# Kernel optimization log

Measured on AMD Instinct MI355X. Metric: run time of the kernel, lower is better.

## Reference

```python
import jax, jax.numpy as jnp
import numpy as np

IMG = 512
STRIDES = (8.0, 16.0, 32.0)   # p3, p4, p5
ROI = 7                        # roi_size
SR = 2                         # roi_align sampling ratio (fixed; torchvision default -1 is adaptive)
IOU_LOW, IOU_HIGH = 0.4, 0.6   # fg/bg matching thresholds (2nd-stage)
NUM_CLASSES = 20
B, R, M, C = 4, 256, 40, 256


def _make_boxes(key, b, n, max_wh):
    k1, k2 = jax.random.split(key)
    cxy = jax.random.uniform(k1, (b, n, 2), minval=0.0, maxval=float(IMG))
    wh = jax.random.uniform(k2, (b, n, 2), minval=16.0, maxval=float(max_wh))
    x1y1 = jnp.clip(cxy - wh / 2, 0.0, IMG - 1.0)
    x2y2 = jnp.clip(cxy + wh / 2, x1y1 + 1.0, float(IMG))
    return jnp.concatenate([x1y1, x2y2], axis=-1)


def setup_inputs() -> dict:
    key = jax.random.key(0)
    ks = jax.random.split(key, 12)
    feats_p3 = jax.random.normal(ks[0], (B, C, 64, 64), jnp.float32)
    feats_p4 = jax.random.normal(ks[1], (B, C, 32, 32), jnp.float32)
    feats_p5 = jax.random.normal(ks[2], (B, C, 16, 16), jnp.float32)
    props_p3 = _make_boxes(ks[3], B, R, 128)
    props_p4 = _make_boxes(ks[4], B, R, 256)
    props_p5 = _make_boxes(ks[5], B, R, 512)
    gt_xyxy = _make_boxes(ks[6], B, M, 400)
    gt_cls = jax.random.randint(ks[7], (B, M, 1), 0, NUM_CLASSES).astype(jnp.float32)
    gt = jnp.concatenate([gt_xyxy, gt_cls], axis=-1)
    pad = (jnp.arange(M) >= 25)[None, :, None]   # last 15 rows are padding (class -1)
    gt_boxes = jnp.where(pad, -1.0, gt)
    conv_w = jax.random.normal(ks[8], (C, C, 3, 3), jnp.float32) * 0.01
    conv_b = jnp.zeros((C,), jnp.float32)
    fc_w = jax.random.normal(ks[9], (NUM_CLASSES + 1, C * ROI * ROI), jnp.float32) * 0.01
    fc_b = jnp.zeros((NUM_CLASSES + 1,), jnp.float32)
    return {"feats_p3": feats_p3, "feats_p4": feats_p4, "feats_p5": feats_p5,
            "props_p3": props_p3, "props_p4": props_p4, "props_p5": props_p5,
            "gt_boxes": gt_boxes, "conv_w": conv_w, "conv_b": conv_b,
            "fc_w": fc_w, "fc_b": fc_b}


def _bilinear(feat, ys, xs):
    # feat: (C,H,W); ys: (R,G,1); xs: (R,1,G) -> (C,R,G,G)
    Cc, H, W = feat.shape
    valid = (ys >= -1.0) & (ys <= H) & (xs >= -1.0) & (xs <= W)
    y = jnp.clip(ys, 0.0, H - 1.0)
    x = jnp.clip(xs, 0.0, W - 1.0)
    y0f = jnp.floor(y); x0f = jnp.floor(x)
    y0 = y0f.astype(jnp.int32); x0 = x0f.astype(jnp.int32)
    y1 = jnp.minimum(y0 + 1, H - 1); x1 = jnp.minimum(x0 + 1, W - 1)
    ly = y - y0f; lx = x - x0f
    hy = 1.0 - ly; hx = 1.0 - lx
    v = (feat[:, y0, x0] * (hy * hx) + feat[:, y0, x1] * (hy * lx)
         + feat[:, y1, x0] * (ly * hx) + feat[:, y1, x1] * (ly * lx))
    return jnp.where(valid, v, 0.0)


def _roi_align(feat, rois, scale):
    # feat: (C,H,W); rois: (R,4) xyxy in image coords; aligned=True
    r = rois.shape[0]
    x1 = rois[:, 0] * scale - 0.5
    y1 = rois[:, 1] * scale - 0.5
    roi_w = rois[:, 2] * scale - 0.5 - x1
    roi_h = rois[:, 3] * scale - 0.5 - y1
    G = ROI * SR
    frac = (jnp.arange(G, dtype=feat.dtype) + 0.5) / G
    xs = x1[:, None] + frac[None, :] * roi_w[:, None]   # (R,G)
    ys = y1[:, None] + frac[None, :] * roi_h[:, None]
    v = _bilinear(feat, ys[:, :, None], xs[:, None, :])  # (C,R,G,G)
    v = v.transpose(1, 0, 2, 3).reshape(r, -1, ROI, SR, ROI, SR)
    return v.mean(axis=(3, 5))                            # (R,C,7,7)


def _iou(b1, b2):
    # b1: (N,4), b2: (M,4) -> (N,M)
    tl = jnp.maximum(b1[:, None, :2], b2[None, :, :2])
    br = jnp.minimum(b1[:, None, 2:4], b2[None, :, 2:4])
    inter = jnp.clip(br - tl, 0.0).prod(-1)
    a1 = (b1[:, 2:4] - b1[:, :2]).prod(-1)
    a2 = (b2[:, 2:4] - b2[:, :2]).prod(-1)
    return inter / (a1[:, None] + a2[None, :] - inter)


def _match(props, gt):
    # props: (N,4); gt: (M,5) padded with class -1
    valid = gt[:, 4] != -1
    m = jnp.where(valid[None, :], _iou(props, gt[:, :4]), -1.0)
    q = m.max(axis=1)
    matched = gt[m.argmax(axis=1)]                       # (N,5)
    matched = jnp.where((q <= IOU_LOW)[:, None], -1.0, matched)      # background
    matched = jnp.where(((q > IOU_LOW) & (q < IOU_HIGH))[:, None], -1e8, matched)  # neutral
    return matched


def reference(feats_p3, feats_p4, feats_p5, props_p3, props_p4, props_p5,
              gt_boxes, conv_w, conv_b, fc_w, fc_b):
    levels = [(feats_p3, props_p3, STRIDES[0]),
              (feats_p4, props_p4, STRIDES[1]),
              (feats_p5, props_p5, STRIDES[2])]
    # ROI-align every proposal at its level; order: image-major, then level, then roi
    per_level = [jax.vmap(lambda f, p, s=s: _roi_align(f, p, 1.0 / s))(f, p)
                 for f, p, s in levels]                   # each (B,R,C,7,7)
    roi_feats = jnp.stack(per_level, axis=1).reshape(-1, C, ROI, ROI)
    # cls head: conv3x3 + relu + flatten + linear
    h = jax.lax.conv_general_dilated(roi_feats, conv_w, (1, 1), 'SAME')
    h = jax.nn.relu(h + conv_b[None, :, None, None])
    logits = h.reshape(h.shape[0], -1) @ fc_w.T + fc_b    # (B*3*R, num_classes+1)
    # match concatenated per-image proposals to GT (no-grad pipeline)
    props_all = jnp.concatenate([props_p3, props_p4, props_p5], axis=1)  # (B,3R,4)
    matched = jax.vmap(_match)(jax.lax.stop_gradient(props_all), gt_boxes)
    return logits, matched
```

## Files before the change

### kernel.cpp

```cpp
#include <hip/hip_runtime.h>

typedef unsigned short ushort_t;
typedef __attribute__((ext_vector_type(4))) unsigned short ushort4_t;
typedef __attribute__((ext_vector_type(8))) short short8;
typedef __attribute__((ext_vector_type(4))) unsigned int uint4v;
typedef __attribute__((ext_vector_type(2))) float float2v;
typedef __attribute__((ext_vector_type(4))) float floatx4;
typedef __attribute__((ext_vector_type(16))) float floatx16;

#define B_ 4
#define C_ 256
#define R_ 256
#define M_ 40
#define NCLS 21
#define ROI_ 7
#define G_ 14
#define NROI_TOT 3072
#define PROPS_PER_IMG 768
#define POOL_PITCH 264
#define WCONV_ELEMS (256 * 2304)
#define NKB 392
#define WFC2_ELEMS (NKB * 32 * 32)
#define OFF_FWB   WCONV_ELEMS
#define OFF_CL3   (OFF_FWB + WFC2_ELEMS)
#define OFF_CL4   (OFF_CL3 + 4 * 64 * 64 * 256)
#define OFF_CL5   (OFF_CL4 + 4 * 32 * 32 * 256)

__device__ __forceinline__ ushort_t f2bf(float f) {
  unsigned u = __builtin_bit_cast(unsigned, f);
  u += 0x7fff + ((u >> 16) & 1);
  return (ushort_t)(u >> 16);
}
__device__ __forceinline__ float bf2f(ushort_t h) {
  unsigned u = ((unsigned)h) << 16;
  return __builtin_bit_cast(float, u);
}
__device__ __forceinline__ float2v cvt2(unsigned u) {
  float2v r;
  r[0] = __builtin_bit_cast(float, u << 16);
  r[1] = __builtin_bit_cast(float, u & 0xffff0000u);
  return r;
}

__global__ __launch_bounds__(256) void prep_kernel(
    const float* __restrict__ cw, const float* __restrict__ fw,
    const float* __restrict__ f3, const float* __restrict__ f4,
    const float* __restrict__ f5, const float* __restrict__ p3,
    const float* __restrict__ p4, const float* __restrict__ p5,
    const float* __restrict__ gt, ushort_t* __restrict__ wr,
    ushort_t* __restrict__ fwb, ushort_t* __restrict__ cl3,
    ushort_t* __restrict__ cl4, ushort_t* __restrict__ cl5,
    float* __restrict__ out) {
  __shared__ ushort_t tile[256 * 65];
  const int id = blockIdx.x;
  const int t = threadIdx.x;

  if (id < 512) {
    const int i0 = id * 256 + t;
    const int stride = 512 * 256;
    for (int idx = i0; idx < WCONV_ELEMS; idx += stride) {
      const int kk = idx >> 12;
      const int rem = idx & 4095;
      const int co = rem >> 4;
      const int i = rem & 15;
      const int k = kk * 16 + i;
      const int j = k >> 8;
      const int ci = k & 255;
      wr[idx] = f2bf(cw[(co * 256 + ci) * 9 + j]);
    }
    for (int idx = i0; idx < WFC2_ELEMS; idx += stride) {
      const int kb = idx >> 10;
      const int rem = idx & 1023;
      const int cls = rem >> 5;
      const int koff = rem & 31;
      fwb[idx] =
          (cls < NCLS) ? f2bf(fw[(size_t)cls * 12544 + kb * 32 + koff]) : 0;
    }
  } else if (id < 960) {
    const int fid = id - 512;
    const float* in;
    ushort_t* outp;
    int b, y, W;
    if (fid < 256) { in = f3; outp = cl3; W = 64; b = fid >> 6; y = fid & 63; }
    else if (fid < 384) { in = f4; outp = cl4; W = 32; b = (fid - 256) >> 5; y = (fid - 256) & 31; }
    else { in = f5; outp = cl5; W = 16; b = (fid - 384) >> 4; y = (fid - 384) & 15; }

    for (int idx = t; idx < 256 * W; idx += 256) {
      const int c = idx / W;
      const int x = idx - c * W;
      tile[c * 65 + x] = f2bf(in[((size_t)(b * 256 + c) * W + y) * W + x]);
    }
    __syncthreads();
    ushort_t* orow = outp + ((size_t)(b * W + y) * W) * 256;
    for (int idx = t; idx < W * 64; idx += 256) {
      const int x = idx >> 6;
      const int c4 = (idx & 63) * 4;
      ushort4_t v;
      v[0] = tile[(c4 + 0) * 65 + x];
      v[1] = tile[(c4 + 1) * 65 + x];
      v[2] = tile[(c4 + 2) * 65 + x];
      v[3] = tile[(c4 + 3) * 65 + x];
      *(ushort4_t*)(orow + (size_t)x * 256 + c4) = v;
    }
  } else {
    const int gidx = (id - 960) * 256 + t;
    if (gidx >= NROI_TOT) return;
    const int b = gidx / PROPS_PER_IMG;
    const int i = gidx - b * PROPS_PER_IMG;
    const int lvl = i >> 8;
    const int r = i & 255;
    const float* prop =
        (lvl == 0 ? p3 : (lvl == 1 ? p4 : p5)) + (size_t)(b * R_ + r) * 4;
    const float px1 = prop[0], py1 = prop[1], px2 = prop[2], py2 = prop[3];
    const float a1 = (px2 - px1) * (py2 - py1);
    const float* gtb = gt + (size_t)b * M_ * 5;

    float best = -2.f;
    int bi = 0;
    for (int j = 0; j < M_; ++j) {
      const float gx1 = gtb[j * 5 + 0], gy1 = gtb[j * 5 + 1];
      const float gx2 = gtb[j * 5 + 2], gy2 = gtb[j * 5 + 3];
      const float cls = gtb[j * 5 + 4];
      const float tlx = fmaxf(px1, gx1), tly = fmaxf(py1, gy1);
      const float brx = fminf(px2, gx2), bry = fminf(py2, gy2);
      const float iw = fmaxf(brx - tlx, 0.f), ih = fmaxf(bry - tly, 0.f);
      const float inter = iw * ih;
      const float a2 = (gx2 - gx1) * (gy2 - gy1);
      const float iou = inter / ((a1 + a2) - inter);
      const float m = (cls != -1.0f) ? iou : -1.0f;
      if (m > best) { best = m; bi = j; }
    }
    float o0, o1, o2, o3, o4;
    if (best <= 0.4f) {
      o0 = o1 = o2 = o3 = o4 = -1.0f;
    } else if (best < 0.6f) {
      o0 = o1 = o2 = o3 = o4 = -1e8f;
    } else {
      o0 = gtb[bi * 5 + 0]; o1 = gtb[bi * 5 + 1]; o2 = gtb[bi * 5 + 2];
      o3 = gtb[bi * 5 + 3]; o4 = gtb[bi * 5 + 4];
    }
    float* od = out + (size_t)NROI_TOT * NCLS + (size_t)gidx * 5;
    od[0] = o0; od[1] = o1; od[2] = o2; od[3] = o3; od[4] = o4;
  }
}

__global__ __launch_bounds__(512, 4) void cls_head_kernel(
    const ushort_t* __restrict__ cl3, const ushort_t* __restrict__ cl4,
    const ushort_t* __restrict__ cl5, const float* __restrict__ p3,
    const float* __restrict__ p4, const float* __restrict__ p5,
    const ushort_t* __restrict__ wr, const float* __restrict__ conv_b,
    const ushort_t* __restrict__ fwb, const float* __restrict__ fc_b,
    float* __restrict__ out) {
  __shared__ __align__(16) ushort_t s_pool[2 * 50 * POOL_PITCH];
  __shared__ int s_iy0[28], s_iy1[28], s_ix0[28], s_ix1[28];
  __shared__ float s_ly[28], s_lx[28], s_vy[28], s_vx[28];
  __shared__ float s_fcred[NCLS * 2 * 8];

  const int bid = blockIdx.x;
  const int t = threadIdx.x;

  const int img = (bid & 7) >> 1;
  const int pair = (bid >> 3) * 2 + (bid & 1);
  const int rid0 = img * PROPS_PER_IMG + pair * 2;

  const ushort_t* clb_[2];
  int W_[2];
  const float* prop_[2];
#pragma unroll
  for (int rr = 0; rr < 2; ++rr) {
    const int rid = rid0 + rr;
    const int b = rid / PROPS_PER_IMG;
    const int rem = rid - b * PROPS_PER_IMG;
    const int lvl = rem >> 8;
    const int r = rem & 255;
    const ushort_t* base;
    const float* pp;
    int Wl;
    if (lvl == 0) { base = cl3; pp = p3; Wl = 64; }
    else if (lvl == 1) { base = cl4; pp = p4; Wl = 32; }
    else { base = cl5; pp = p5; Wl = 16; }
    clb_[rr] = base + (size_t)b * Wl * Wl * 256;
    W_[rr] = Wl;
    prop_[rr] = pp + (size_t)(b * R_ + r) * 4;
  }

  if (t < 256) {
    s_pool[49 * POOL_PITCH + t] = 0;
    s_pool[99 * POOL_PITCH + t] = 0;
  }

  if (t < 56) {
    const int rr = t / 28;
    const int tt = t - rr * 28;
    const float* prop = prop_[rr];
    const int H = W_[rr];
    const float scale = 1.0f / (float)(H == 64 ? 8 : (H == 32 ? 16 : 32));
    const float bx1 = prop[0], by1 = prop[1], bx2 = prop[2], by2 = prop[3];
    const float ax = bx1 * scale - 0.5f;
    const float ay = by1 * scale - 0.5f;
    const float rw = bx2 * scale - 0.5f - ax;
    const float rh = by2 * scale - 0.5f - ay;
    const int i = (tt < G_) ? tt : (tt - G_);
    const float frac = ((float)i + 0.5f) / (float)G_;
    const int o = rr * G_ + i;
    if (tt < G_) {
      float yy = ay + frac * rh;
      float v = (yy >= -1.0f && yy <= (float)H) ? 1.0f : 0.0f;
      float y = fminf(fmaxf(yy, 0.0f), (float)(H - 1));
      float y0f = floorf(y);
      int y0 = (int)y0f;
      s_iy0[o] = y0;
      s_iy1[o] = min(y0 + 1, H - 1);
      s_ly[o] = y - y0f;
      s_vy[o] = v;
    } else {
      float xx = ax + frac * rw;
      float v = (xx >= -1.0f && xx <= (float)H) ? 1.0f : 0.0f;
      float x = fminf(fmaxf(xx, 0.0f), (float)(H - 1));
      float x0f = floorf(x);
      int x0 = (int)x0f;
      s_ix0[o] = x0;
      s_ix1[o] = min(x0 + 1, H - 1);
      s_lx[o] = x - x0f;
      s_vx[o] = v;
    }
  }
  __syncthreads();

  const int l = t & 63;
  const int w = t >> 6;

  {
    const int hw = l >> 5;
    const int c8 = (l & 31) * 8;
    for (int cb = w * 2; cb < 98; cb += 16) {
      const int cell = cb + hw;
      if (cell >= 98) continue;
      const int rr = (cell >= 49) ? 1 : 0;
      const int pos = cell - rr * 49;
      const int py = pos / 7, px = pos - (pos / 7) * 7;
      const ushort_t* clb = clb_[rr];
      const int W = W_[rr];
      float2v a01 = {0.f, 0.f}, a23 = {0.f, 0.f};
      float2v a45 = {0.f, 0.f}, a67 = {0.f, 0.f};
#pragma unroll
      for (int sy = 0; sy < 2; ++sy) {
        const int gy = rr * G_ + 2 * py + sy;
        const int iy0 = s_iy0[gy], iy1 = s_iy1[gy];
        const float ly = s_ly[gy], vy = s_vy[gy];
        const float hy = 1.0f - ly;
#pragma unroll
        for (int sx = 0; sx < 2; ++sx) {
          const int gx = rr * G_ + 2 * px + sx;
          const int ix0 = s_ix0[gx], ix1 = s_ix1[gx];
          const float lx = s_lx[gx], vx = s_vx[gx];
          const float hx = 1.0f - lx;
          const float vv = vy * vx;
          const float w00 = vv * hy * hx, w01 = vv * hy * lx;
          const float w10 = vv * ly * hx, w11 = vv * ly * lx;
          const uint4v u00 = *(const uint4v*)(clb + ((size_t)(iy0 * W + ix0) * 256 + c8));
          const uint4v u01 = *(const uint4v*)(clb + ((size_t)(iy0 * W + ix1) * 256 + c8));
          const uint4v u10 = *(const uint4v*)(clb + ((size_t)(iy1 * W + ix0) * 256 + c8));
          const uint4v u11 = *(const uint4v*)(clb + ((size_t)(iy1 * W + ix1) * 256 + c8));
          a01 += cvt2(u00[0]) * w00 + cvt2(u01[0]) * w01 +
                 cvt2(u10[0]) * w10 + cvt2(u11[0]) * w11;
          a23 += cvt2(u00[1]) * w00 + cvt2(u01[1]) * w01 +
                 cvt2(u10[1]) * w10 + cvt2(u11[1]) * w11;
          a45 += cvt2(u00[2]) * w00 + cvt2(u01[2]) * w01 +
                 cvt2(u10[2]) * w10 + cvt2(u11[2]) * w11;
          a67 += cvt2(u00[3]) * w00 + cvt2(u01[3]) * w01 +
                 cvt2(u10[3]) * w10 + cvt2(u11[3]) * w11;
        }
      }
      short8 pv;
      pv[0] = (short)f2bf(a01[0] * 0.25f);
      pv[1] = (short)f2bf(a01[1] * 0.25f);
      pv[2] = (short)f2bf(a23[0] * 0.25f);
      pv[3] = (short)f2bf(a23[1] * 0.25f);
      pv[4] = (short)f2bf(a45[0] * 0.25f);
      pv[5] = (short)f2bf(a45[1] * 0.25f);
      pv[6] = (short)f2bf(a67[0] * 0.25f);
      pv[7] = (short)f2bf(a67[1] * 0.25f);
      *(short8*)&s_pool[(rr * 50 + pos) * POOL_PITCH + c8] = pv;
    }
  }
  __syncthreads();

  const int ml = l & 31;
  const int quad = l >> 5;
  const int co_base = w * 32;

  const int pA = ml;
  const int pB = ml + 32;
  const int pyA = pA / 7, pxA = pA % 7;
  const int pyB = pB / 7, pxB = pB % 7;

  floatx16 acc[4];
#pragma unroll
  for (int a = 0; a < 4; ++a)
#pragma unroll
    for (int i = 0; i < 16; ++i) acc[a][i] = 0.f;

  const ushort_t* a0p = wr + (co_base + ml) * 16 + quad * 8;

  int kk = 0;
  for (int j = 0; j < 9; ++j) {
    const int dy = j / 3 - 1, dx = j % 3 - 1;
    int bnA, bnB;
    {
      const int ry = pyA + dy, rx = pxA + dx;
      const bool ok = (ry >= 0) & (ry < 7) & (rx >= 0) & (rx < 7);
      bnA = ok ? ry * 7 + rx : 49;
    }
    {
      const int ry = pyB + dy, rx = pxB + dx;
      const bool ok = (pB < 49) & (ry >= 0) & (ry < 7) & (rx >= 0) & (rx < 7);
      bnB = ok ? ry * 7 + rx : 49;
    }
    const int row0 = bnA, row1 = bnB, row2 = 50 + bnA, row3 = 50 + bnB;

#pragma unroll 4
    for (int kc = 0; kc < 16; ++kc, ++kk) {
      const short8 a0 = *(const short8*)(a0p + kk * 4096);
      const int cof = kc * 16 + quad * 8;
      const short8 b0 = *(const short8*)&s_pool[row0 * POOL_PITCH + cof];
      const short8 b1 = *(const short8*)&s_pool[row1 * POOL_PITCH + cof];
      const short8 b2 = *(const short8*)&s_pool[row2 * POOL_PITCH + cof];
      const short8 b3 = *(const short8*)&s_pool[row3 * POOL_PITCH + cof];
      acc[0] = __builtin_amdgcn_mfma_f32_32x32x16_bf16(a0, b0, acc[0], 0, 0, 0);
      acc[1] = __builtin_amdgcn_mfma_f32_32x32x16_bf16(a0, b1, acc[1], 0, 0, 0);
      acc[2] = __builtin_amdgcn_mfma_f32_32x32x16_bf16(a0, b2, acc[2], 0, 0, 0);
      acc[3] = __builtin_amdgcn_mfma_f32_32x32x16_bf16(a0, b3, acc[3], 0, 0, 0);
    }
  }
  __syncthreads();

  ushort_t* h_lds = s_pool;
#pragma unroll
  for (int reg = 0; reg < 16; ++reg) {
    const int co = co_base + (reg & 3) + 8 * (reg >> 2) + 4 * quad;
    const float cb = conv_b[co];
    const int base = co * 49;
    h_lds[base + pA] = f2bf(fmaxf(acc[0][reg] + cb, 0.f));
    h_lds[12544 + base + pA] = f2bf(fmaxf(acc[2][reg] + cb, 0.f));
    if (pB < 49) {
      h_lds[base + pB] = f2bf(fmaxf(acc[1][reg] + cb, 0.f));
      h_lds[12544 + base + pB] = f2bf(fmaxf(acc[3][reg] + cb, 0.f));
    }
  }
  __syncthreads();

  {
    const int n = l & 15;
    const int kq = l >> 4;
    const ushort_t* ap0 = fwb + (n * 4 + kq) * 8;
    const ushort_t* ap1 = ap0 + 512;
    const ushort_t* bp = h_lds + (size_t)(l & 1) * 12544 + kq * 8;
    const int kb0 = w * 49;

    floatx4 fa0, fa1;
#pragma unroll
    for (int i = 0; i < 4; ++i) { fa0[i] = 0.f; fa1[i] = 0.f; }

    for (int it = 0; it < 49; ++it) {
      const int kb = kb0 + it;
      const short8 av0 = *(const short8*)(ap0 + kb * 1024);
      const short8 av1 = *(const short8*)(ap1 + kb * 1024);
      const short8 bv = *(const short8*)(bp + kb * 32);
      fa0 = __builtin_amdgcn_mfma_f32_16x16x32_bf16(av0, bv, fa0, 0, 0, 0);
      fa1 = __builtin_amdgcn_mfma_f32_16x16x32_bf16(av1, bv, fa1, 0, 0, 0);
    }
    if (n < 2) {
      const int m4 = kq * 4;
#pragma unroll
      for (int reg = 0; reg < 4; ++reg) {
        const int cls0 = m4 + reg;
        const int cls1 = 16 + m4 + reg;
        s_fcred[(cls0 * 2 + n) * 8 + w] = fa0[reg];
        if (cls1 < NCLS) s_fcred[(cls1 * 2 + n) * 8 + w] = fa1[reg];
      }
    }
  }
  __syncthreads();
  if (t < 2 * NCLS) {
    const int cls = t >> 1;
    const int rr = t & 1;
    const float* pr = &s_fcred[(cls * 2 + rr) * 8];
    float s = pr[0] + pr[1] + pr[2] + pr[3] + pr[4] + pr[5] + pr[6] + pr[7];
    out[(size_t)(rid0 + rr) * NCLS + cls] = s + fc_b[cls];
  }
}

extern "C" void kernel_launch(void* const* d_in, const int* in_sizes, int n_in,
                              void* d_out, int out_size, void* d_ws,
                              size_t ws_size, hipStream_t stream) {
  const float* f3 = (const float*)d_in[0];
  const float* f4 = (const float*)d_in[1];
  const float* f5 = (const float*)d_in[2];
  const float* p3 = (const float*)d_in[3];
  const float* p4 = (const float*)d_in[4];
  const float* p5 = (const float*)d_in[5];
  const float* gt = (const float*)d_in[6];
  const float* cw = (const float*)d_in[7];
  const float* cb = (const float*)d_in[8];
  const float* fw = (const float*)d_in[9];
  const float* fb = (const float*)d_in[10];
  float* out = (float*)d_out;

  ushort_t* wsp = (ushort_t*)d_ws;
  ushort_t* wr = wsp;
  ushort_t* fwb = wsp + OFF_FWB;
  ushort_t* cl3 = wsp + OFF_CL3;
  ushort_t* cl4 = wsp + OFF_CL4;
  ushort_t* cl5 = wsp + OFF_CL5;

  prep_kernel<<<972, 256, 0, stream>>>(cw, fw, f3, f4, f5, p3, p4, p5, gt, wr,
                                       fwb, cl3, cl4, cl5, out);
  cls_head_kernel<<<NROI_TOT / 2, 512, 0, stream>>>(cl3, cl4, cl5, p3, p4, p5,
                                                    wr, cb, fwb, fb, out);
}
```

Before: 357.0 us.

## Process one ROI per block in cls head and vectorize feature transpose loads

The classification head kernel now handles a single ROI per block instead of two. That halves LDS pooling storage and MFMA accumulators, and raises the launch-bounds occupancy hint from 4 to 6 with twice as many blocks. The trade-off is that each block re-streams the full conv and FC weights for only one ROI, which doubles weight traffic, and the FC MFMA wastes its spare columns. Separately, the prep kernel's NCHW-to-NHWC transpose now reads features with float4 loads and writes packed bf16 into a 68-pitch LDS tile.

```diff
diff --git a/kernel.cpp b/kernel.cpp
--- a/kernel.cpp
+++ b/kernel.cpp
@@ -51,7 +51,7 @@
     ushort_t* __restrict__ fwb, ushort_t* __restrict__ cl3,
     ushort_t* __restrict__ cl4, ushort_t* __restrict__ cl5,
     float* __restrict__ out) {
-  __shared__ ushort_t tile[256 * 65];
+  __shared__ ushort_t tile[256 * 68];
   const int id = blockIdx.x;
   const int t = threadIdx.x;
 
@@ -85,10 +85,18 @@
     else if (fid < 384) { in = f4; outp = cl4; W = 32; b = (fid - 256) >> 5; y = (fid - 256) & 31; }
     else { in = f5; outp = cl5; W = 16; b = (fid - 384) >> 4; y = (fid - 384) & 15; }
 
-    for (int idx = t; idx < 256 * W; idx += 256) {
-      const int c = idx / W;
-      const int x = idx - c * W;
-      tile[c * 65 + x] = f2bf(in[((size_t)(b * 256 + c) * W + y) * W + x]);
+    const int W4 = W >> 2;
+    for (int idx = t; idx < 256 * W4; idx += 256) {
+      const int c = idx / W4;
+      const int x4 = (idx - c * W4) * 4;
+      const float4 v =
+          *(const float4*)&in[((size_t)(b * 256 + c) * W + y) * W + x4];
+      ushort4_t u;
+      u[0] = f2bf(v.x);
+      u[1] = f2bf(v.y);
+      u[2] = f2bf(v.z);
+      u[3] = f2bf(v.w);
+      *(ushort4_t*)&tile[c * 68 + x4] = u;
     }
     __syncthreads();
     ushort_t* orow = outp + ((size_t)(b * W + y) * W) * 256;
@@ -96,10 +104,10 @@
       const int x = idx >> 6;
       const int c4 = (idx & 63) * 4;
       ushort4_t v;
-      v[0] = tile[(c4 + 0) * 65 + x];
-      v[1] = tile[(c4 + 1) * 65 + x];
-      v[2] = tile[(c4 + 2) * 65 + x];
-      v[3] = tile[(c4 + 3) * 65 + x];
+      v[0] = tile[(c4 + 0) * 68 + x];
+      v[1] = tile[(c4 + 1) * 68 + x];
+      v[2] = tile[(c4 + 2) * 68 + x];
+      v[3] = tile[(c4 + 3) * 68 + x];
       *(ushort4_t*)(orow + (size_t)x * 256 + c4) = v;
     }
   } else {
@@ -144,85 +152,67 @@
   }
 }
 
-__global__ __launch_bounds__(512, 4) void cls_head_kernel(
+__global__ __launch_bounds__(512, 6) void cls_head_kernel(
     const ushort_t* __restrict__ cl3, const ushort_t* __restrict__ cl4,
     const ushort_t* __restrict__ cl5, const float* __restrict__ p3,
     const float* __restrict__ p4, const float* __restrict__ p5,
     const ushort_t* __restrict__ wr, const float* __restrict__ conv_b,
     const ushort_t* __restrict__ fwb, const float* __restrict__ fc_b,
     float* __restrict__ out) {
-  __shared__ __align__(16) ushort_t s_pool[2 * 50 * POOL_PITCH];
-  __shared__ int s_iy0[28], s_iy1[28], s_ix0[28], s_ix1[28];
-  __shared__ float s_ly[28], s_lx[28], s_vy[28], s_vx[28];
-  __shared__ float s_fcred[NCLS * 2 * 8];
+  __shared__ __align__(16) ushort_t s_pool[50 * POOL_PITCH];
+  __shared__ int s_iy0[G_], s_iy1[G_], s_ix0[G_], s_ix1[G_];
+  __shared__ float s_ly[G_], s_lx[G_], s_vy[G_], s_vx[G_];
+  __shared__ float s_fcred[NCLS * 8];
 
   const int bid = blockIdx.x;
   const int t = threadIdx.x;
 
   const int img = (bid & 7) >> 1;
-  const int pair = (bid >> 3) * 2 + (bid & 1);
-  const int rid0 = img * PROPS_PER_IMG + pair * 2;
-
-  const ushort_t* clb_[2];
-  int W_[2];
-  const float* prop_[2];
-#pragma unroll
-  for (int rr = 0; rr < 2; ++rr) {
-    const int rid = rid0 + rr;
-    const int b = rid / PROPS_PER_IMG;
-    const int rem = rid - b * PROPS_PER_IMG;
-    const int lvl = rem >> 8;
-    const int r = rem & 255;
-    const ushort_t* base;
-    const float* pp;
-    int Wl;
-    if (lvl == 0) { base = cl3; pp = p3; Wl = 64; }
-    else if (lvl == 1) { base = cl4; pp = p4; Wl = 32; }
-    else { base = cl5; pp = p5; Wl = 16; }
-    clb_[rr] = base + (size_t)b * Wl * Wl * 256;
-    W_[rr] = Wl;
-    prop_[rr] = pp + (size_t)(b * R_ + r) * 4;
-  }
-
-  if (t < 256) {
-    s_pool[49 * POOL_PITCH + t] = 0;
-    s_pool[99 * POOL_PITCH + t] = 0;
-  }
-
-  if (t < 56) {
-    const int rr = t / 28;
-    const int tt = t - rr * 28;
-    const float* prop = prop_[rr];
-    const int H = W_[rr];
-    const float scale = 1.0f / (float)(H == 64 ? 8 : (H == 32 ? 16 : 32));
+  const int roi = (bid >> 3) * 2 + (bid & 1);
+  const int rid = img * PROPS_PER_IMG + roi;
+
+  const int lvl = roi >> 8;
+  const int r = roi & 255;
+  const ushort_t* clb;
+  const float* pp;
+  int W;
+  if (lvl == 0) { clb = cl3; pp = p3; W = 64; }
+  else if (lvl == 1) { clb = cl4; pp = p4; W = 32; }
+  else { clb = cl5; pp = p5; W = 16; }
+  clb += (size_t)img * W * W * 256;
+  const float* prop = pp + (size_t)(img * R_ + r) * 4;
+
+  if (t < 256) s_pool[49 * POOL_PITCH + t] = 0;
+
+  if (t < 2 * G_) {
+    const float scale = 1.0f / (float)(W == 64 ? 8 : (W == 32 ? 16 : 32));
     const float bx1 = prop[0], by1 = prop[1], bx2 = prop[2], by2 = prop[3];
     const float ax = bx1 * scale - 0.5f;
     const float ay = by1 * scale - 0.5f;
     const float rw = bx2 * scale - 0.5f - ax;
     const float rh = by2 * scale - 0.5f - ay;
-    const int i = (tt < G_) ? tt : (tt - G_);
+    const int i = (t < G_) ? t : (t - G_);
     const float frac = ((float)i + 0.5f) / (float)G_;
-    const int o = rr * G_ + i;
-    if (tt < G_) {
+    if (t < G_) {
       float yy = ay + frac * rh;
-      float v = (yy >= -1.0f && yy <= (float)H) ? 1.0f : 0.0f;
-      float y = fminf(fmaxf(yy, 0.0f), (float)(H - 1));
+      float v = (yy >= -1.0f && yy <= (float)W) ? 1.0f : 0.0f;
+      float y = fminf(fmaxf(yy, 0.0f), (float)(W - 1));
       float y0f = floorf(y);
       int y0 = (int)y0f;
-      s_iy0[o] = y0;
-      s_iy1[o] = min(y0 + 1, H - 1);
-      s_ly[o] = y - y0f;
-      s_vy[o] = v;
+      s_iy0[i] = y0;
+      s_iy1[i] = min(y0 + 1, W - 1);
+      s_ly[i] = y - y0f;
+      s_vy[i] = v;
     } else {
       float xx = ax + frac * rw;
-      float v = (xx >= -1.0f && xx <= (float)H) ? 1.0f : 0.0f;
-      float x = fminf(fmaxf(xx, 0.0f), (float)(H - 1));
+      float v = (xx >= -1.0f && xx <= (float)W) ? 1.0f : 0.0f;
+      float x = fminf(fmaxf(xx, 0.0f), (float)(W - 1));
       float x0f = floorf(x);
       int x0 = (int)x0f;
-      s_ix0[o] = x0;
-      s_ix1[o] = min(x0 + 1, H - 1);
-      s_lx[o] = x - x0f;
-      s_vx[o] = v;
+      s_ix0[i] = x0;
+      s_ix1[i] = min(x0 + 1, W - 1);
+      s_lx[i] = x - x0f;
+      s_vx[i] = v;
     }
   }
   __syncthreads();
@@ -233,25 +223,21 @@
   {
     const int hw = l >> 5;
     const int c8 = (l & 31) * 8;
-    for (int cb = w * 2; cb < 98; cb += 16) {
+    for (int cb = w * 2; cb < 49; cb += 16) {
       const int cell = cb + hw;
-      if (cell >= 98) continue;
-      const int rr = (cell >= 49) ? 1 : 0;
-      const int pos = cell - rr * 49;
-      const int py = pos / 7, px = pos - (pos / 7) * 7;
-      const ushort_t* clb = clb_[rr];
-      const int W = W_[rr];
+      if (cell >= 49) continue;
+      const int py = cell / 7, px = cell - (cell / 7) * 7;
       float2v a01 = {0.f, 0.f}, a23 = {0.f, 0.f};
       float2v a45 = {0.f, 0.f}, a67 = {0.f, 0.f};
 #pragma unroll
       for (int sy = 0; sy < 2; ++sy) {
-        const int gy = rr * G_ + 2 * py + sy;
+        const int gy = 2 * py + sy;
         const int iy0 = s_iy0[gy], iy1 = s_iy1[gy];
         const float ly = s_ly[gy], vy = s_vy[gy];
         const float hy = 1.0f - ly;
 #pragma unroll
         for (int sx = 0; sx < 2; ++sx) {
-          const int gx = rr * G_ + 2 * px + sx;
+          const int gx = 2 * px + sx;
           const int ix0 = s_ix0[gx], ix1 = s_ix1[gx];
           const float lx = s_lx[gx], vx = s_vx[gx];
           const float hx = 1.0f - lx;
@@ -281,7 +267,7 @@
       pv[5] = (short)f2bf(a45[1] * 0.25f);
       pv[6] = (short)f2bf(a67[0] * 0.25f);
       pv[7] = (short)f2bf(a67[1] * 0.25f);
-      *(short8*)&s_pool[(rr * 50 + pos) * POOL_PITCH + c8] = pv;
+      *(short8*)&s_pool[cell * POOL_PITCH + c8] = pv;
     }
   }
   __syncthreads();
@@ -295,11 +281,9 @@
   const int pyA = pA / 7, pxA = pA % 7;
   const int pyB = pB / 7, pxB = pB % 7;
 
-  floatx16 acc[4];
-#pragma unroll
-  for (int a = 0; a < 4; ++a)
-#pragma unroll
-    for (int i = 0; i < 16; ++i) acc[a][i] = 0.f;
+  floatx16 acc0, acc1;
+#pragma unroll
+  for (int i = 0; i < 16; ++i) { acc0[i] = 0.f; acc1[i] = 0.f; }
 
   const ushort_t* a0p = wr + (co_base + ml) * 16 + quad * 8;
 
@@ -317,20 +301,15 @@
       const bool ok = (pB < 49) & (ry >= 0) & (ry < 7) & (rx >= 0) & (rx < 7);
       bnB = ok ? ry * 7 + rx : 49;
     }
-    const int row0 = bnA, row1 = bnB, row2 = 50 + bnA, row3 = 50 + bnB;
 
 #pragma unroll 4
     for (int kc = 0; kc < 16; ++kc, ++kk) {
       const short8 a0 = *(const short8*)(a0p + kk * 4096);
       const int cof = kc * 16 + quad * 8;
-      const short8 b0 = *(const short8*)&s_pool[row0 * POOL_PITCH + cof];
-      const short8 b1 = *(const short8*)&s_pool[row1 * POOL_PITCH + cof];
-      const short8 b2 = *(const short8*)&s_pool[row2 * POOL_PITCH + cof];
-      const short8 b3 = *(const short8*)&s_pool[row3 * POOL_PITCH + cof];
-      acc[0] = __builtin_amdgcn_mfma_f32_32x32x16_bf16(a0, b0, acc[0], 0, 0, 0);
-      acc[1] = __builtin_amdgcn_mfma_f32_32x32x16_bf16(a0, b1, acc[1], 0, 0, 0);
-      acc[2] = __builtin_amdgcn_mfma_f32_32x32x16_bf16(a0, b2, acc[2], 0, 0, 0);
-      acc[3] = __builtin_amdgcn_mfma_f32_32x32x16_bf16(a0, b3, acc[3], 0, 0, 0);
+      const short8 b0 = *(const short8*)&s_pool[bnA * POOL_PITCH + cof];
+      const short8 b1 = *(const short8*)&s_pool[bnB * POOL_PITCH + cof];
+      acc0 = __builtin_amdgcn_mfma_f32_32x32x16_bf16(a0, b0, acc0, 0, 0, 0);
+      acc1 = __builtin_amdgcn_mfma_f32_32x32x16_bf16(a0, b1, acc1, 0, 0, 0);
     }
   }
   __syncthreads();
@@ -341,12 +320,8 @@
     const int co = co_base + (reg & 3) + 8 * (reg >> 2) + 4 * quad;
     const float cb = conv_b[co];
     const int base = co * 49;
-    h_lds[base + pA] = f2bf(fmaxf(acc[0][reg] + cb, 0.f));
-    h_lds[12544 + base + pA] = f2bf(fmaxf(acc[2][reg] + cb, 0.f));
-    if (pB < 49) {
-      h_lds[base + pB] = f2bf(fmaxf(acc[1][reg] + cb, 0.f));
-      h_lds[12544 + base + pB] = f2bf(fmaxf(acc[3][reg] + cb, 0.f));
-    }
+    h_lds[base + pA] = f2bf(fmaxf(acc0[reg] + cb, 0.f));
+    if (pB < 49) h_lds[base + pB] = f2bf(fmaxf(acc1[reg] + cb, 0.f));
   }
   __syncthreads();
 
@@ -355,7 +330,7 @@
     const int kq = l >> 4;
     const ushort_t* ap0 = fwb + (n * 4 + kq) * 8;
     const ushort_t* ap1 = ap0 + 512;
-    const ushort_t* bp = h_lds + (size_t)(l & 1) * 12544 + kq * 8;
+    const ushort_t* bp = h_lds + kq * 8;
     const int kb0 = w * 49;
 
     floatx4 fa0, fa1;
@@ -370,24 +345,22 @@
       fa0 = __builtin_amdgcn_mfma_f32_16x16x32_bf16(av0, bv, fa0, 0, 0, 0);
       fa1 = __builtin_amdgcn_mfma_f32_16x16x32_bf16(av1, bv, fa1, 0, 0, 0);
     }
-    if (n < 2) {
+    if (n == 0) {
       const int m4 = kq * 4;
 #pragma unroll
       for (int reg = 0; reg < 4; ++reg) {
         const int cls0 = m4 + reg;
         const int cls1 = 16 + m4 + reg;
-        s_fcred[(cls0 * 2 + n) * 8 + w] = fa0[reg];
-        if (cls1 < NCLS) s_fcred[(cls1 * 2 + n) * 8 + w] = fa1[reg];
+        s_fcred[cls0 * 8 + w] = fa0[reg];
+        if (cls1 < NCLS) s_fcred[cls1 * 8 + w] = fa1[reg];
       }
     }
   }
   __syncthreads();
-  if (t < 2 * NCLS) {
-    const int cls = t >> 1;
-    const int rr = t & 1;
-    const float* pr = &s_fcred[(cls * 2 + rr) * 8];
+  if (t < NCLS) {
+    const float* pr = &s_fcred[t * 8];
     float s = pr[0] + pr[1] + pr[2] + pr[3] + pr[4] + pr[5] + pr[6] + pr[7];
-    out[(size_t)(rid0 + rr) * NCLS + cls] = s + fc_b[cls];
+    out[(size_t)rid * NCLS + t] = s + fc_b[t];
   }
 }
 
@@ -416,6 +389,6 @@
 
   prep_kernel<<<972, 256, 0, stream>>>(cw, fw, f3, f4, f5, p3, p4, p5, gt, wr,
                                        fwb, cl3, cl4, cl5, out);
-  cls_head_kernel<<<NROI_TOT / 2, 512, 0, stream>>>(cl3, cl4, cl5, p3, p4, p5,
-                                                    wr, cb, fwb, fb, out);
-}
+  cls_head_kernel<<<NROI_TOT, 512, 0, stream>>>(cl3, cl4, cl5, p3, p4, p5, wr,
+                                                cb, fwb, fb, out);
+}
```

Result: slower. 435.6 us (+22.0%).
